# Optimization experiments

Hardware: AMD Instinct MI355X
Metric: run time of the kernel (lower is better)

Reference implementation:

```python
import jax, jax.numpy as jnp
import numpy as np

RES = 1024
NUM_ROOMS = 8
N_AGENTS = 5_000_000


def setup_inputs() -> dict:
    key = jax.random.key(0)
    k1, k2, k3 = jax.random.split(key, 3)
    agent_positions = jax.random.uniform(k1, (N_AGENTS, 2), dtype=jnp.float32)
    room_params = jax.random.uniform(k2, (NUM_ROOMS, 4), dtype=jnp.float32)
    # torch init: params[:, 2:] = params[:, 2:] * 0.1 + 0.05  (room sigmas)
    room_params = room_params.at[:, 2:].set(room_params[:, 2:] * 0.1 + 0.05)
    wall_density = jax.random.uniform(k3, (RES, RES), dtype=jnp.float32)
    return {
        "agent_positions": agent_positions,
        "room_params": room_params,
        "wall_density": wall_density,
    }


def reference(agent_positions, room_params, wall_density):
    res = wall_density.shape[0]
    lin = jnp.linspace(0.0, 1.0, res, dtype=wall_density.dtype)
    x_grid, y_grid = jnp.meshgrid(lin, lin, indexing="ij")  # [res,res]

    # Per-room Gaussian density maps, vectorized over rooms -> [R,res,res]
    cx = room_params[:, 0, None, None]
    cy = room_params[:, 1, None, None]
    sx = room_params[:, 2, None, None]
    sy = room_params[:, 3, None, None]
    spatial_layout = jnp.exp(
        -((x_grid - cx) ** 2 / (2.0 * sx**2) + (y_grid - cy) ** 2 / (2.0 * sy**2))
    )

    # Agent flow histogram via single fused scatter-add
    ix = jnp.clip((agent_positions[:, 0] * res).astype(jnp.int32), 0, res - 1)
    iy = jnp.clip((agent_positions[:, 1] * res).astype(jnp.int32), 0, res - 1)
    flow_field = jnp.zeros((res, res), dtype=wall_density.dtype).at[ix, iy].add(1.0)
    flow_field = flow_field / (flow_field.max() + 1e-6)

    dynamic_layout = spatial_layout * (1.0 - wall_density[None, :, :])
    return (dynamic_layout, flow_field)
```

## Files before the change

### kernel.cpp

```cpp
#include <hip/hip_runtime.h>

#define RES 1024
#define NROOMS 8
#define NBUCKETS 256
#define BINS_PER_BUCKET (4 * RES)
#define CAP 32768
#define SWPB 8
#define NBLK 512
#define F4PT 10
#define AGB_MAX (NBLK * 2 * F4PT)
#define STG_MAX (512 * F4PT * 2)

typedef unsigned int u32x4 __attribute__((ext_vector_type(4)));

__device__ __forceinline__ void dyn_cell(
    const float* __restrict__ room_params,
    const float4* __restrict__ wall,
    float4* __restrict__ dyn, int idx)
{
    int i  = idx >> 8;
    int j0 = (idx & 255) << 2;
    const float inv1023 = 1.0f / 1023.0f;
    float x  = (float)i * inv1023;
    float y0 = (float)(j0 + 0) * inv1023;
    float y1 = (float)(j0 + 1) * inv1023;
    float y2 = (float)(j0 + 2) * inv1023;
    float y3 = (float)(j0 + 3) * inv1023;

    float4 w = wall[idx];
    float omx = 1.0f - w.x;
    float omy = 1.0f - w.y;
    float omz = 1.0f - w.z;
    float omw = 1.0f - w.w;

    const int plane4 = (RES * RES) / 4;
    #pragma unroll
    for (int r = 0; r < NROOMS; ++r) {
        float cx = room_params[4 * r + 0];
        float cy = room_params[4 * r + 1];
        float sx = room_params[4 * r + 2];
        float sy = room_params[4 * r + 3];
        float isx = 1.0f / (2.0f * sx * sx);
        float isy = 1.0f / (2.0f * sy * sy);
        float dx = x - cx;
        float ax = dx * dx * isx;
        float d0 = y0 - cy, d1 = y1 - cy, d2 = y2 - cy, d3 = y3 - cy;
        float4 d;
        d.x = __expf(-(ax + d0 * d0 * isy)) * omx;
        d.y = __expf(-(ax + d1 * d1 * isy)) * omy;
        d.z = __expf(-(ax + d2 * d2 * isy)) * omz;
        d.w = __expf(-(ax + d3 * d3 * isy)) * omw;
        dyn[(size_t)r * plane4 + idx] = d;
    }
}

__global__ __launch_bounds__(512) void scatter_kernel(
    const float4* __restrict__ pos, int n4, int nagents,
    unsigned short* __restrict__ buf, unsigned int* __restrict__ cursor,
    const float* __restrict__ room_params,
    const float4* __restrict__ wall,
    float4* __restrict__ dyn)
{
    __shared__ unsigned int   cnt[SWPB][NBUCKETS];
    __shared__ unsigned int   sbase[SWPB][NBUCKETS];
    __shared__ unsigned int   pstart[NBUCKETS];
    __shared__ unsigned int   ptotal[NBUCKETS];
    __shared__ unsigned int   gbase[NBUCKETS];
    __shared__ unsigned int   wsum[4];
    __shared__ unsigned short staged[STG_MAX];

    int tid  = threadIdx.x;
    int wv   = tid >> 6;
    int lane = tid & 63;

    #pragma unroll
    for (int i = 0; i < (SWPB * NBUCKETS) / 512; ++i)
        ((unsigned int*)cnt)[tid + 512 * i] = 0u;
    __syncthreads();

    int chunk = (n4 + NBLK - 1) / NBLK;
    int start = blockIdx.x * chunk;
    int end   = min(start + chunk, n4);

    unsigned int   code[2 * F4PT];
    unsigned short rank[2 * F4PT];
    #pragma unroll
    for (int k = 0; k < F4PT; ++k) {
        int i4 = start + (k << 9) + tid;
        if (i4 < end) {
            float4 p = pos[i4];
            int ix0 = min(max((int)(p.x * 1024.0f), 0), 1023);
            int iy0 = min(max((int)(p.y * 1024.0f), 0), 1023);
            int ix1 = min(max((int)(p.z * 1024.0f), 0), 1023);
            int iy1 = min(max((int)(p.w * 1024.0f), 0), 1023);
            unsigned int b0 = (unsigned int)(ix0 >> 2);
            unsigned int b1 = (unsigned int)(ix1 >> 2);
            code[2 * k]     = (b0 << 16) | (unsigned int)(((ix0 & 3) << 10) | iy0);
            code[2 * k + 1] = (b1 << 16) | (unsigned int)(((ix1 & 3) << 10) | iy1);
            rank[2 * k]     = (unsigned short)atomicAdd(&cnt[wv][b0], 1u);
            rank[2 * k + 1] = (unsigned short)atomicAdd(&cnt[wv][b1], 1u);
        } else {
            code[2 * k] = 0xFFFFFFFFu;
            code[2 * k + 1] = 0xFFFFFFFFu;
        }
    }
    __syncthreads();

    if (tid < NBUCKETS) {
        unsigned int run = 0;
        #pragma unroll
        for (int w = 0; w < SWPB; ++w) {
            unsigned int c = cnt[w][tid];
            sbase[w][tid] = run;
            run += c;
        }
        ptotal[tid] = run;
        gbase[tid]  = run ? atomicAdd(&cursor[tid], run) : 0u;
        unsigned int t = run;
        #pragma unroll
        for (int off = 1; off < 64; off <<= 1) {
            unsigned int v = (unsigned int)__shfl_up((int)t, off, 64);
            if (lane >= off) t += v;
        }
        if (lane == 63) wsum[wv] = t;
        pstart[tid] = t - run;
    }
    __syncthreads();
    if (tid < NBUCKETS) {
        unsigned int off = 0;
        #pragma unroll
        for (int w = 0; w < 3; ++w) if (w < wv) off += wsum[w];
        unsigned int ps = pstart[tid] + off;
        pstart[tid] = ps;
        #pragma unroll
        for (int w = 0; w < SWPB; ++w) sbase[w][tid] += ps;
    }
    __syncthreads();

    #pragma unroll
    for (int k = 0; k < 2 * F4PT; ++k) {
        unsigned int cd = code[k];
        if (cd != 0xFFFFFFFFu) {
            unsigned int b = cd >> 16;
            staged[sbase[wv][b] + rank[k]] = (unsigned short)(cd & 0xFFFFu);
        }
    }
    __syncthreads();

    #pragma unroll 4
    for (int bb = 0; bb < 32; ++bb) {
        int b = (wv << 5) + bb;
        unsigned int n  = ptotal[b];
        unsigned int ps = pstart[b];
        unsigned int gb = gbase[b];
        for (unsigned int e = lane; e < n; e += 64) {
            unsigned int p = gb + e;
            if (p < CAP) buf[b * CAP + p] = staged[ps + e];
        }
    }

    dyn_cell(room_params, wall, dyn, blockIdx.x * 512 + tid);

    if (blockIdx.x == 0 && tid == 0 && (nagents & 1)) {
        const float* t = (const float*)pos;
        float px = t[2 * (nagents - 1)];
        float py = t[2 * (nagents - 1) + 1];
        int ix = min(max((int)(px * 1024.0f), 0), 1023);
        int iy = min(max((int)(py * 1024.0f), 0), 1023);
        unsigned int b = (unsigned int)(ix >> 2);
        unsigned int p = atomicAdd(&cursor[b], 1u);
        if (p < CAP) buf[b * CAP + p] = (unsigned short)(((ix & 3) << 10) | iy);
    }
}

__global__ __launch_bounds__(1024) void hist_build_kernel(
    const unsigned short* __restrict__ buf,
    const unsigned int* __restrict__ cursor,
    unsigned int* __restrict__ counts,
    unsigned int* __restrict__ out_max)
{
    __shared__ __align__(16) unsigned int h[BINS_PER_BUCKET];
    int b = blockIdx.x, tid = threadIdx.x;
    #pragma unroll
    for (int i = 0; i < BINS_PER_BUCKET / 1024; ++i) h[tid + 1024 * i] = 0u;
    __syncthreads();

    unsigned int n = min(cursor[b], (unsigned int)CAP);
    const unsigned short* seg = buf + (size_t)b * CAP;
    unsigned int n2 = n & ~1u;
    for (unsigned int i = 2 * tid; i < n2; i += 2048) {
        unsigned int u = *(const unsigned int*)(seg + i);
        atomicAdd(&h[u & 0xFFFFu], 1u);
        atomicAdd(&h[u >> 16], 1u);
    }
    if (tid == 0 && (n & 1)) atomicAdd(&h[seg[n - 1]], 1u);
    __syncthreads();

    u32x4 v = ((const u32x4*)h)[tid];
    ((u32x4*)counts)[(size_t)b * (BINS_PER_BUCKET / 4) + tid] = v;
    unsigned int m = max(max(v.x, v.y), max(v.z, v.w));
    #pragma unroll
    for (int off = 32; off > 0; off >>= 1)
        m = max(m, (unsigned int)__shfl_down((int)m, off, 64));
    __shared__ unsigned int sm[16];
    if ((tid & 63) == 0) sm[tid >> 6] = m;
    __syncthreads();
    if (tid == 0) {
        #pragma unroll
        for (int w = 1; w < 16; ++w) m = max(m, sm[w]);
        atomicMax(out_max, m);
    }
}

__global__ __launch_bounds__(256) void norm_kernel(
    float* __restrict__ flow, const unsigned int* __restrict__ maxp)
{
    int idx = blockIdx.x * blockDim.x + threadIdx.x;
    uint4 c = ((const uint4*)flow)[idx];
    float inv = 1.0f / ((float)(*maxp) + 1e-6f);
    ((float4*)flow)[idx] = make_float4((float)c.x * inv, (float)c.y * inv,
                                       (float)c.z * inv, (float)c.w * inv);
}

__global__ __launch_bounds__(256) void hist_atomic_kernel(
    const float4* __restrict__ pos, int n4, int nagents,
    unsigned int* __restrict__ counts)
{
    int idx = blockIdx.x * blockDim.x + threadIdx.x;
    int stride = gridDim.x * blockDim.x;
    for (int i = idx; i < n4; i += stride) {
        float4 p = pos[i];
        int ix0 = min(max((int)(p.x * 1024.0f), 0), 1023);
        int iy0 = min(max((int)(p.y * 1024.0f), 0), 1023);
        int ix1 = min(max((int)(p.z * 1024.0f), 0), 1023);
        int iy1 = min(max((int)(p.w * 1024.0f), 0), 1023);
        atomicAdd(&counts[(ix0 << 10) + iy0], 1u);
        atomicAdd(&counts[(ix1 << 10) + iy1], 1u);
    }
    if (idx == 0 && (nagents & 1)) {
        const float* t = (const float*)pos;
        int ix = min(max((int)(t[2 * (nagents - 1)] * 1024.0f), 0), 1023);
        int iy = min(max((int)(t[2 * (nagents - 1) + 1] * 1024.0f), 0), 1023);
        atomicAdd(&counts[(ix << 10) + iy], 1u);
    }
}

__global__ __launch_bounds__(256) void max_kernel(
    const uint4* __restrict__ counts, unsigned int* __restrict__ out_max)
{
    int idx = blockIdx.x * blockDim.x + threadIdx.x;
    int stride = gridDim.x * blockDim.x;
    unsigned int m = 0;
    const int n4 = (RES * RES) / 4;
    for (int i = idx; i < n4; i += stride) {
        uint4 c = counts[i];
        m = max(m, max(max(c.x, c.y), max(c.z, c.w)));
    }
    #pragma unroll
    for (int off = 32; off > 0; off >>= 1)
        m = max(m, (unsigned int)__shfl_down((int)m, off, 64));
    __shared__ unsigned int sm[4];
    if ((threadIdx.x & 63) == 0) sm[threadIdx.x >> 6] = m;
    __syncthreads();
    if (threadIdx.x == 0) {
        m = max(max(sm[0], sm[1]), max(sm[2], sm[3]));
        atomicMax(out_max, m);
    }
}

__global__ __launch_bounds__(256) void final_full_kernel(
    const float* __restrict__ room_params,
    const float4* __restrict__ wall,
    float4* __restrict__ dyn,
    float* __restrict__ flow,
    const unsigned int* __restrict__ maxp)
{
    int idx = blockIdx.x * blockDim.x + threadIdx.x;
    uint4 c = ((const uint4*)flow)[idx];
    float inv = 1.0f / ((float)(*maxp) + 1e-6f);
    ((float4*)flow)[idx] = make_float4((float)c.x * inv, (float)c.y * inv,
                                       (float)c.z * inv, (float)c.w * inv);
    dyn_cell(room_params, wall, dyn, idx);
}

extern "C" void kernel_launch(void* const* d_in, const int* in_sizes, int n_in,
                              void* d_out, int out_size, void* d_ws, size_t ws_size,
                              hipStream_t stream) {
    const float* agents      = (const float*)d_in[0];
    const float* room_params = (const float*)d_in[1];
    const float* wall        = (const float*)d_in[2];

    float* dyn  = (float*)d_out;
    float* flow = (float*)d_out + (size_t)NROOMS * RES * RES;
    unsigned int* counts = (unsigned int*)flow;

    int nagents = in_sizes[0] / 2;
    int n4 = nagents / 2;

    size_t need = 2048 + (size_t)NBUCKETS * CAP * sizeof(unsigned short);

    bool fits = ((n4 + NBLK - 1) / NBLK) <= (F4PT * 512);

    if (ws_size >= need && fits) {
        unsigned int*   cursor = (unsigned int*)d_ws;
        unsigned int*   maxp   = (unsigned int*)((char*)d_ws + 1024);
        unsigned short* buf    = (unsigned short*)((char*)d_ws + 2048);

        (void)hipMemsetAsync(d_ws, 0, 2048, stream);
        scatter_kernel<<<NBLK, 512, 0, stream>>>(
            (const float4*)agents, n4, nagents, buf, cursor,
            room_params, (const float4*)wall, (float4*)dyn);
        hist_build_kernel<<<NBUCKETS, 1024, 0, stream>>>(buf, cursor, counts, maxp);
        norm_kernel<<<(RES * RES / 4) / 256, 256, 0, stream>>>(flow, maxp);
    } else {
        unsigned int* maxp = (unsigned int*)d_ws;
        (void)hipMemsetAsync(flow, 0, (size_t)RES * RES * sizeof(float), stream);
        (void)hipMemsetAsync(maxp, 0, sizeof(unsigned int), stream);
        hist_atomic_kernel<<<1280, 256, 0, stream>>>((const float4*)agents, n4, nagents, counts);
        max_kernel<<<256, 256, 0, stream>>>((const uint4*)counts, maxp);
        final_full_kernel<<<(RES * RES / 4) / 256, 256, 0, stream>>>(
            room_params, (const float4*)wall, (float4*)dyn, flow, maxp);
    }
}
```

Baseline: 121.7 us.

## Spill per-thread codes to LDS, reuse count array, overlap dyn writes, nontemporal stores

Per-thread code/rank arrays are packed into one 32-bit word (bucket, rank, bin) and kept in shared memory instead of registers, and the sbase array is folded into cnt. The launch bounds now request 4 blocks per SM to raise occupancy. The dense dynamic-layout computation moves before the first barrier so its stores overlap the scatter phase, and those stores become nontemporal. This adds LDS traffic and about 40KB of extra shared memory, which may itself cap occupancy. The packing also relies on per-wave bucket ranks staying below 2048.

New measurement: 118.4 us. 1.03x faster.

```diff
diff --git a/kernel.cpp b/kernel.cpp
--- a/kernel.cpp
+++ b/kernel.cpp
@@ -8,10 +8,10 @@
 #define SWPB 8
 #define NBLK 512
 #define F4PT 10
-#define AGB_MAX (NBLK * 2 * F4PT)
 #define STG_MAX (512 * F4PT * 2)
 
 typedef unsigned int u32x4 __attribute__((ext_vector_type(4)));
+typedef float        f32x4 __attribute__((ext_vector_type(4)));
 
 __device__ __forceinline__ void dyn_cell(
     const float* __restrict__ room_params,
@@ -45,16 +45,17 @@
         float dx = x - cx;
         float ax = dx * dx * isx;
         float d0 = y0 - cy, d1 = y1 - cy, d2 = y2 - cy, d3 = y3 - cy;
-        float4 d;
+        f32x4 d;
         d.x = __expf(-(ax + d0 * d0 * isy)) * omx;
         d.y = __expf(-(ax + d1 * d1 * isy)) * omy;
         d.z = __expf(-(ax + d2 * d2 * isy)) * omz;
         d.w = __expf(-(ax + d3 * d3 * isy)) * omw;
-        dyn[(size_t)r * plane4 + idx] = d;
-    }
-}
-
-__global__ __launch_bounds__(512) void scatter_kernel(
+        __builtin_nontemporal_store(
+            d, reinterpret_cast<f32x4*>(&dyn[(size_t)r * plane4 + idx]));
+    }
+}
+
+__global__ __launch_bounds__(512, 4) void scatter_kernel(
     const float4* __restrict__ pos, int n4, int nagents,
     unsigned short* __restrict__ buf, unsigned int* __restrict__ cursor,
     const float* __restrict__ room_params,
@@ -62,12 +63,12 @@
     float4* __restrict__ dyn)
 {
     __shared__ unsigned int   cnt[SWPB][NBUCKETS];
-    __shared__ unsigned int   sbase[SWPB][NBUCKETS];
     __shared__ unsigned int   pstart[NBUCKETS];
     __shared__ unsigned int   ptotal[NBUCKETS];
     __shared__ unsigned int   gbase[NBUCKETS];
     __shared__ unsigned int   wsum[4];
     __shared__ unsigned short staged[STG_MAX];
+    __shared__ unsigned int   codeLDS[2 * F4PT][512];
 
     int tid  = threadIdx.x;
     int wv   = tid >> 6;
@@ -82,8 +83,6 @@
     int start = blockIdx.x * chunk;
     int end   = min(start + chunk, n4);
 
-    unsigned int   code[2 * F4PT];
-    unsigned short rank[2 * F4PT];
     #pragma unroll
     for (int k = 0; k < F4PT; ++k) {
         int i4 = start + (k << 9) + tid;
@@ -95,15 +94,20 @@
             int iy1 = min(max((int)(p.w * 1024.0f), 0), 1023);
             unsigned int b0 = (unsigned int)(ix0 >> 2);
             unsigned int b1 = (unsigned int)(ix1 >> 2);
-            code[2 * k]     = (b0 << 16) | (unsigned int)(((ix0 & 3) << 10) | iy0);
-            code[2 * k + 1] = (b1 << 16) | (unsigned int)(((ix1 & 3) << 10) | iy1);
-            rank[2 * k]     = (unsigned short)atomicAdd(&cnt[wv][b0], 1u);
-            rank[2 * k + 1] = (unsigned short)atomicAdd(&cnt[wv][b1], 1u);
+            unsigned int bin0 = (unsigned int)(((ix0 & 3) << 10) | iy0);
+            unsigned int bin1 = (unsigned int)(((ix1 & 3) << 10) | iy1);
+            unsigned int r0 = atomicAdd(&cnt[wv][b0], 1u);
+            unsigned int r1 = atomicAdd(&cnt[wv][b1], 1u);
+            codeLDS[2 * k][tid]     = (b0 << 23) | (r0 << 12) | bin0;
+            codeLDS[2 * k + 1][tid] = (b1 << 23) | (r1 << 12) | bin1;
         } else {
-            code[2 * k] = 0xFFFFFFFFu;
-            code[2 * k + 1] = 0xFFFFFFFFu;
-        }
-    }
+            codeLDS[2 * k][tid]     = 0xFFFFFFFFu;
+            codeLDS[2 * k + 1][tid] = 0xFFFFFFFFu;
+        }
+    }
+
+    dyn_cell(room_params, wall, dyn, blockIdx.x * 512 + tid);
+
     __syncthreads();
 
     if (tid < NBUCKETS) {
@@ -111,7 +115,7 @@
         #pragma unroll
         for (int w = 0; w < SWPB; ++w) {
             unsigned int c = cnt[w][tid];
-            sbase[w][tid] = run;
+            cnt[w][tid] = run;
             run += c;
         }
         ptotal[tid] = run;
@@ -133,16 +137,18 @@
         unsigned int ps = pstart[tid] + off;
         pstart[tid] = ps;
         #pragma unroll
-        for (int w = 0; w < SWPB; ++w) sbase[w][tid] += ps;
+        for (int w = 0; w < SWPB; ++w) cnt[w][tid] += ps;
     }
     __syncthreads();
 
     #pragma unroll
     for (int k = 0; k < 2 * F4PT; ++k) {
-        unsigned int cd = code[k];
-        if (cd != 0xFFFFFFFFu) {
-            unsigned int b = cd >> 16;
-            staged[sbase[wv][b] + rank[k]] = (unsigned short)(cd & 0xFFFFu);
+        unsigned int u = codeLDS[k][tid];
+        if (u != 0xFFFFFFFFu) {
+            unsigned int b   = u >> 23;
+            unsigned int r   = (u >> 12) & 0x7FFu;
+            unsigned int bin = u & 0xFFFu;
+            staged[cnt[wv][b] + r] = (unsigned short)bin;
         }
     }
     __syncthreads();
@@ -158,8 +164,6 @@
             if (p < CAP) buf[b * CAP + p] = staged[ps + e];
         }
     }
-
-    dyn_cell(room_params, wall, dyn, blockIdx.x * 512 + tid);
 
     if (blockIdx.x == 0 && tid == 0 && (nagents & 1)) {
         const float* t = (const float*)pos;
```
